# Optimization experiments

Hardware: AMD Instinct MI355X
Metric: run time of the kernel (lower is better)

The kernel has to match this reference:

```python
import jax, jax.numpy as jnp
import numpy as np
from jax import lax

NUM_ENT = 100000
NUM_REL = 500
ENT_DIM = 100   # emb_dim1 * emb_dim2 = 10 * 10
REL_DIM = 2500  # 100 filters * 5 * 5
BATCH = 1024
EPS = 1e-5


def _bn(x, gamma, beta, axes):
    # training-mode batchnorm (batch statistics), matching torch BN in train mode
    mean = jnp.mean(x, axis=axes, keepdims=True)
    var = jnp.var(x, axis=axes, keepdims=True)
    shape = [1] * x.ndim
    ch_axis = [a for a in range(x.ndim) if a not in axes][0]
    shape[ch_axis] = x.shape[ch_axis]
    g = gamma.reshape(shape)
    b = beta.reshape(shape)
    return (x - mean) * g * lax.rsqrt(var + EPS) + b


def setup_inputs() -> dict:
    key = jax.random.key(0)
    ks = jax.random.split(key, 6)
    e1 = jax.random.randint(ks[0], (BATCH,), 0, NUM_ENT)
    rel = jax.random.randint(ks[1], (BATCH,), 0, NUM_REL)
    emb_e = jax.random.normal(ks[2], (NUM_ENT, ENT_DIM), jnp.float32) * 0.1
    emb_rel = jax.random.normal(ks[3], (NUM_REL, REL_DIM), jnp.float32) * 0.1
    fc_w = jax.random.normal(ks[4], (ENT_DIM, 100 * 6 * 6), jnp.float32) * 0.02
    fc_b = jnp.zeros((ENT_DIM,), jnp.float32)
    bias = jnp.zeros((NUM_ENT,), jnp.float32)
    return {
        "e1": e1, "rel": rel,
        "emb_e": emb_e, "emb_rel": emb_rel,
        "fc_w": fc_w, "fc_b": fc_b, "bias": bias,
        "g0": jnp.ones((1,), jnp.float32), "b0": jnp.zeros((1,), jnp.float32),
        "g1": jnp.ones((100,), jnp.float32), "b1": jnp.zeros((100,), jnp.float32),
        "grel": jnp.ones((REL_DIM,), jnp.float32), "brel": jnp.zeros((REL_DIM,), jnp.float32),
        "g2": jnp.ones((ENT_DIM,), jnp.float32), "b2": jnp.zeros((ENT_DIM,), jnp.float32),
    }


def reference(e1, rel, emb_e, emb_rel, fc_w, fc_b, bias, g0, b0, g1, b1, grel, brel, g2, b2):
    B = e1.shape[0]
    e = emb_e[e1].reshape(B, 1, 10, 10)          # [B,1,10,10]
    r = emb_rel[rel]                              # [B,2500]
    r = _bn(r, grel, brel, axes=(0,))
    e = _bn(e, g0, b0, axes=(0, 2, 3))
    # dropout layers are identity (inference)
    filters = r.reshape(B * 100, 1, 5, 5)         # per-sample dynamic filters
    # per-sample conv as a single grouped conv: groups = B
    x = lax.conv_general_dilated(
        e.reshape(1, B, 10, 10), filters,
        window_strides=(1, 1), padding='VALID',
        feature_group_count=B,
        dimension_numbers=('NCHW', 'OIHW', 'NCHW'))
    x = x.reshape(B, 100, 6, 6)
    x = jax.nn.relu(_bn(x, g1, b1, axes=(0, 2, 3)))
    x = x.reshape(B, -1) @ fc_w.T + fc_b          # [B,100]
    x = jax.nn.relu(_bn(x, g2, b2, axes=(0,)))
    logits = x @ emb_e.T + bias                   # [B,NUM_ENT] memory-bound
    return jax.nn.sigmoid(logits)
```

## Files before the change

### kernel.cpp

```cpp
#include <hip/hip_runtime.h>
#include <cstdint>

#define NENT 100000
#define EPS 1e-5f

constexpr long REL_A    = 0;
constexpr long REL_B    = 2500;
constexpr long EPART    = 5000;
constexpr long EAB      = 5040;
constexpr long A1O      = 5056;
constexpr long C1O      = 5156;
constexpr long PART_OFF = 5888;
constexpr long XBUF_OFF = 415488;
constexpr long XHAT_OFF = 4101888;
constexpr long PSTAT    = XBUF_OFF;

typedef __attribute__((ext_vector_type(8))) __bf16 bf16x8;
typedef __attribute__((ext_vector_type(4))) float  f32x4;

#define BARLK() asm volatile("s_waitcnt lgkmcnt(0)\n\ts_barrier" ::: "memory")

__device__ __forceinline__ unsigned short f2bf(float f) {
    unsigned int u = __float_as_uint(f);
    unsigned int r = (u + 0x7FFFu + ((u >> 16) & 1u)) >> 16;
    return (unsigned short)r;
}

__global__ void k_stats1(const int* __restrict__ rel, const float* __restrict__ emb_rel,
                         const int* __restrict__ e1, const float* __restrict__ emb_e,
                         float* __restrict__ ws) {
    __shared__ float shmem[512];
    int tid = threadIdx.x, blk = blockIdx.x;
    if (blk < 125) {
        int* cnti = (int*)shmem;
        for (int i = tid; i < 512; i += 256) cnti[i] = 0;
        __syncthreads();
        for (int i = tid; i < 1024; i += 256) atomicAdd(&cnti[rel[i]], 1);
        __syncthreads();
        float s[10], q[10];
#pragma unroll
        for (int k = 0; k < 10; k++) { s[k] = 0.f; q[k] = 0.f; }
#pragma unroll
        for (int rr = 0; rr < 4; rr++) {
            int r = blk * 4 + rr;
            float c = (float)cnti[r];
            if (c != 0.f) {
                const float* row = emb_rel + (long)r * 2500;
#pragma unroll
                for (int k = 0; k < 10; k++) {
                    int idx = tid + k * 256;
                    if (idx < 2500) {
                        float v = row[idx];
                        s[k] = fmaf(c, v, s[k]);
                        q[k] = fmaf(c * v, v, q[k]);
                    }
                }
            }
        }
        float* ps = ws + PSTAT + (long)blk * 5000;
#pragma unroll
        for (int k = 0; k < 10; k++) {
            int idx = tid + k * 256;
            if (idx < 2500) { ps[idx] = s[k]; ps[2500 + idx] = q[k]; }
        }
    } else if (blk < 141) {
        float* ps = shmem;
        __shared__ float pq[256];
        __shared__ int eidx[64];
        int bi = blk - 125;
        if (tid < 64) eidx[tid] = e1[bi * 64 + tid];
        __syncthreads();
        float s = 0.f, q = 0.f;
        for (int i = tid; i < 6400; i += 256) {
            int b = i / 100, d = i - b * 100;
            float v = emb_e[(long)eidx[b] * 100 + d];
            s += v; q += v * v;
        }
        ps[tid] = s; pq[tid] = q;
        __syncthreads();
        for (int off = 128; off > 0; off >>= 1) {
            if (tid < off) { ps[tid] += ps[tid + off]; pq[tid] += pq[tid + off]; }
            __syncthreads();
        }
        if (tid == 0) { ws[EPART + bi * 2] = ps[0]; ws[EPART + bi * 2 + 1] = pq[0]; }
    }
}

__global__ void k_stats2(const float* __restrict__ grel, const float* __restrict__ brel,
                         const float* __restrict__ g0, const float* __restrict__ b0,
                         float* __restrict__ ws) {
    __shared__ float ps[512], pq[512];
    int tid = threadIdx.x, blk = blockIdx.x;
    if (blk < 40) {
        int f = blk * 64 + (tid & 63);
        int g = tid >> 6;
        float s = 0.f, q = 0.f;
        for (int p = g; p < 125; p += 8) {
            s += ws[PSTAT + (long)p * 5000 + f];
            q += ws[PSTAT + (long)p * 5000 + 2500 + f];
        }
        ps[tid] = s; pq[tid] = q;
        __syncthreads();
        if (tid < 64) {
            float ss = 0.f, qq = 0.f;
#pragma unroll
            for (int k = 0; k < 8; k++) { ss += ps[tid + k * 64]; qq += pq[tid + k * 64]; }
            float mean = ss * (1.f / 1024.f);
            float var  = qq * (1.f / 1024.f) - mean * mean;
            float a = grel[f] * rsqrtf(var + EPS);
            ws[REL_A + f] = a;
            ws[REL_B + f] = brel[f] - mean * a;
        }
    } else if (tid == 0) {
        float s = 0.f, q = 0.f;
#pragma unroll
        for (int i = 0; i < 16; i++) { s += ws[EPART + 2 * i]; q += ws[EPART + 2 * i + 1]; }
        float mean = s * (1.f / 102400.f);
        float var  = q * (1.f / 102400.f) - mean * mean;
        float a = g0[0] * rsqrtf(var + EPS);
        ws[EAB]     = a;
        ws[EAB + 1] = b0[0] - mean * a;
    }
}

__global__ void k_conv(const int* __restrict__ e1, const int* __restrict__ rel,
                       const float* __restrict__ emb_e, const float* __restrict__ emb_rel,
                       const float* __restrict__ ws, float* __restrict__ xout,
                       float* __restrict__ bn1part) {
    __shared__ float es[100];
    __shared__ float flt[2500];
    __shared__ float prs[600], prq[600];
    int b = blockIdx.x, tid = threadIdx.x;
    float a0 = ws[EAB], c0 = ws[EAB + 1];
    long ebase = (long)e1[b] * 100;
    for (int i = tid; i < 100; i += 256) es[i] = a0 * emb_e[ebase + i] + c0;
    long rbase = (long)rel[b] * 2500;
    for (int i = tid; i < 2500; i += 256) flt[i] = ws[REL_A + i] * emb_rel[rbase + i] + ws[REL_B + i];
    __syncthreads();
    for (int u = tid; u < 600; u += 256) {
        int f = u / 6, oi = u - f * 6;
        float er[5][10];
#pragma unroll
        for (int p = 0; p < 5; p++)
#pragma unroll
            for (int c = 0; c < 10; c++) er[p][c] = es[(oi + p) * 10 + c];
        float fw[25];
#pragma unroll
        for (int k = 0; k < 25; k++) fw[k] = flt[f * 25 + k];
        float* dst = xout + (long)b * 3600 + f * 36 + oi * 6;
        float s6 = 0.f, q6 = 0.f;
#pragma unroll
        for (int oj = 0; oj < 6; oj++) {
            float acc = 0.f;
#pragma unroll
            for (int p = 0; p < 5; p++)
#pragma unroll
                for (int q = 0; q < 5; q++) acc += er[p][oj + q] * fw[p * 5 + q];
            dst[oj] = acc;
            s6 += acc; q6 = fmaf(acc, acc, q6);
        }
        prs[u] = s6; prq[u] = q6;
    }
    __syncthreads();
    if (tid < 100) {
        float s = 0.f, q = 0.f;
#pragma unroll
        for (int k = 0; k < 6; k++) { s += prs[tid * 6 + k]; q += prq[tid * 6 + k]; }
        bn1part[(long)b * 200 + tid]       = s;
        bn1part[(long)b * 200 + 100 + tid] = q;
    }
}

__global__ void k_bn1r(const float* __restrict__ bn1part, const float* __restrict__ g1,
                       const float* __restrict__ b1, float* __restrict__ ws) {
    __shared__ float ps[256], pq[256];
    int f = blockIdx.x, tid = threadIdx.x;
    float s = 0.f, q = 0.f;
    for (int b = tid; b < 1024; b += 256) {
        s += bn1part[(long)b * 200 + f];
        q += bn1part[(long)b * 200 + 100 + f];
    }
    ps[tid] = s; pq[tid] = q;
    __syncthreads();
    for (int off = 128; off > 0; off >>= 1) {
        if (tid < off) { ps[tid] += ps[tid + off]; pq[tid] += pq[tid + off]; }
        __syncthreads();
    }
    if (tid == 0) {
        float mean = ps[0] * (1.f / 36864.f);
        float var  = pq[0] * (1.f / 36864.f) - mean * mean;
        float a = g1[f] * rsqrtf(var + EPS);
        ws[A1O + f] = a;
        ws[C1O + f] = b1[f] - mean * a;
    }
}

__global__ void k_fc(const float* __restrict__ xbuf, const float* __restrict__ fc_w,
                     const float* __restrict__ ws, float* __restrict__ part) {
    __shared__ float a1s[100], c1s[100];
    __shared__ float xs[4][900];
    int tid = threadIdx.x;
    int sb = blockIdx.x, kc = blockIdx.y;
    if (tid < 100) { a1s[tid] = ws[A1O + tid]; c1s[tid] = ws[C1O + tid]; }
    __syncthreads();
    int b0s = sb * 4, k0 = kc * 900;
    for (int idx = tid; idx < 3600; idx += 256) {
        int s = idx / 900, k = idx - s * 900;
        int kg = k0 + k;
        int f = kg / 36;
        float v = xbuf[(long)(b0s + s) * 3600 + kg];
        v = a1s[f] * v + c1s[f];
        xs[s][k] = v > 0.f ? v : 0.f;
    }
    __syncthreads();
    if (tid < 200) {
        int j = tid % 100, sg = tid / 100;
        float acc0 = 0.f, acc1 = 0.f;
        const float4* wrow = (const float4*)(fc_w + (long)j * 3600 + k0);
        const float4* x0 = (const float4*)(&xs[sg][0]);
        const float4* x1 = (const float4*)(&xs[sg + 2][0]);
#pragma unroll 5
        for (int kk = 0; kk < 225; kk++) {
            float4 w4 = wrow[kk];
            float4 a4 = x0[kk], b4 = x1[kk];
            acc0 += w4.x * a4.x + w4.y * a4.y + w4.z * a4.z + w4.w * a4.w;
            acc1 += w4.x * b4.x + w4.y * b4.y + w4.z * b4.z + w4.w * b4.w;
        }
        part[((long)kc * 1024 + b0s + sg) * 100 + j]     = acc0;
        part[((long)kc * 1024 + b0s + sg + 2) * 100 + j] = acc1;
    }
}

__global__ void k_bn2x(const float* __restrict__ part, const float* __restrict__ fc_b,
                       const float* __restrict__ g2, const float* __restrict__ b2,
                       unsigned short* __restrict__ xhat) {
    int j = blockIdx.x, tid = threadIdx.x;
    if (j >= 100) {
        for (int t = 0; t < 4; t++) xhat[(long)(tid + t * 256) * 128 + j] = 0;
        return;
    }
    __shared__ float ps[256], pq[256];
    __shared__ float ab[2];
    float v[4];
    float s = 0.f, q = 0.f;
#pragma unroll
    for (int t = 0; t < 4; t++) {
        int b = tid + t * 256;
        float x = part[(long)b * 100 + j] + part[(long)(1024 + b) * 100 + j]
                + part[(long)(2048 + b) * 100 + j] + part[(long)(3072 + b) * 100 + j]
                + fc_b[j];
        v[t] = x; s += x; q += x * x;
    }
    ps[tid] = s; pq[tid] = q;
    __syncthreads();
    for (int off = 128; off > 0; off >>= 1) {
        if (tid < off) { ps[tid] += ps[tid + off]; pq[tid] += pq[tid + off]; }
        __syncthreads();
    }
    if (tid == 0) {
        float mean = ps[0] * (1.f / 1024.f);
        float var  = pq[0] * (1.f / 1024.f) - mean * mean;
        float a = g2[j] * rsqrtf(var + EPS);
        ab[0] = a; ab[1] = b2[j] - mean * a;
    }
    __syncthreads();
    float a = ab[0], c = ab[1];
#pragma unroll
    for (int t = 0; t < 4; t++) {
        float x = a * v[t] + c;
        x = x > 0.f ? x : 0.f;
        xhat[(long)(tid + t * 256) * 128 + j] = f2bf(x);
    }
}

__global__ void __launch_bounds__(256, 2)
k_gemm(const unsigned short* __restrict__ xhat, const float* __restrict__ emb_e,
       const float* __restrict__ bias, float* __restrict__ out) {
    __shared__ __align__(16) unsigned short Es[256 * 128];
    char* EsB = (char*)Es;
    int tid = threadIdx.x;
    int n0 = blockIdx.x * 256;

    {
        int r = tid;
        int g = n0 + r;
        unsigned int rowb = (unsigned)r * 256u;
        unsigned int sw = ((unsigned)r & 7u) << 4;
        ushort4 z; z.x = z.y = z.z = z.w = 0;
        if (g < NENT) {
            const float4* src = (const float4*)(emb_e + (long)g * 100);
#pragma unroll
            for (int i = 0; i < 25; i++) {
                float4 v = src[i];
                ushort4 h;
                h.x = f2bf(v.x); h.y = f2bf(v.y); h.z = f2bf(v.z); h.w = f2bf(v.w);
                *(ushort4*)(EsB + ((rowb + 8u * i) ^ sw)) = h;
            }
        } else {
#pragma unroll
            for (int i = 0; i < 25; i++) *(ushort4*)(EsB + ((rowb + 8u * i) ^ sw)) = z;
        }
#pragma unroll
        for (int zz = 0; zz < 7; zz++) *(ushort4*)(EsB + ((rowb + 200u + 8u * zz) ^ sw)) = z;
    }
    __syncthreads();

    int w = tid >> 6, l = tid & 63;
    int l15 = l & 15, l4 = l >> 4;

    bf16x8 Af[4][4];
#pragma unroll
    for (int fe = 0; fe < 4; fe++) {
        unsigned int r = (unsigned)(w * 64 + fe * 16 + l15);
        unsigned int base = r * 256u + (unsigned)(l4 * 16);
        unsigned int sw = (r & 7u) << 4;
#pragma unroll
        for (int ks = 0; ks < 4; ks++)
            Af[ks][fe] = *(const bf16x8*)(EsB + ((base + (unsigned)(ks * 64)) ^ sw));
    }
    BARLK();

    int colg = n0 + l * 4;
    bool colv = colg < NENT;
    f32x4 bb = colv ? *(const f32x4*)(bias + colg) : f32x4{0.f, 0.f, 0.f, 0.f};

    int xrow = l15 * 128 + l4 * 8;

    bf16x8 Bp[4];
#pragma unroll
    for (int fx = 0; fx < 4; fx++)
        Bp[fx] = *(const bf16x8*)(xhat + (long)(fx * 2048 + xrow));

    for (int chunk = 0; chunk < 16; ++chunk) {
        int m0 = chunk * 64;
        f32x4 acc[4][4];
#pragma unroll
        for (int fe = 0; fe < 4; fe++)
#pragma unroll
            for (int fx = 0; fx < 4; fx++) acc[fe][fx] = f32x4{0.f, 0.f, 0.f, 0.f};

#pragma unroll
        for (int fe = 0; fe < 4; fe++)
#pragma unroll
            for (int fx = 0; fx < 4; fx++)
                acc[fe][fx] = __builtin_amdgcn_mfma_f32_16x16x32_bf16(Af[0][fe], Bp[fx], acc[fe][fx], 0, 0, 0);

#pragma unroll
        for (int ks = 1; ks < 4; ++ks) {
            bf16x8 Bf[4];
#pragma unroll
            for (int fx = 0; fx < 4; fx++)
                Bf[fx] = *(const bf16x8*)(xhat + (long)(m0 * 128 + fx * 2048 + ks * 32 + xrow));
#pragma unroll
            for (int fe = 0; fe < 4; fe++)
#pragma unroll
                for (int fx = 0; fx < 4; fx++)
                    acc[fe][fx] = __builtin_amdgcn_mfma_f32_16x16x32_bf16(Af[ks][fe], Bf[fx], acc[fe][fx], 0, 0, 0);
        }

        if (chunk < 15) {
            int m0n = (chunk + 1) * 64;
#pragma unroll
            for (int fx = 0; fx < 4; fx++)
                Bp[fx] = *(const bf16x8*)(xhat + (long)(m0n * 128 + fx * 2048 + xrow));
        }

#pragma unroll
        for (int fe = 0; fe < 4; fe++) {
            unsigned int s = (unsigned)(w * 16 + fe * 4 + l4);
#pragma unroll
            for (int fx = 0; fx < 4; fx++) {
                unsigned int row = (unsigned)(fx * 16 + l15);
                *(f32x4*)(EsB + row * 1024u + ((s ^ (row & 7u)) * 16u)) = acc[fe][fx];
            }
        }
        BARLK();

#pragma unroll
        for (int pass = 0; pass < 16; pass++) {
            unsigned int row = (unsigned)(pass * 4 + w);
            f32x4 v = *(f32x4*)(EsB + row * 1024u + ((((unsigned)l) ^ (row & 7u)) * 16u));
            f32x4 o;
#pragma unroll
            for (int k = 0; k < 4; k++) {
                float x = v[k] + bb[k];
                float e = __builtin_amdgcn_exp2f(x * -1.44269504f);
                o[k] = __builtin_amdgcn_rcpf(1.0f + e);
            }
            if (colv)
                __builtin_nontemporal_store(o, (f32x4*)(out + (long)(m0 + row) * NENT + colg));
        }
        BARLK();
    }
}

extern "C" void kernel_launch(void* const* d_in, const int* in_sizes, int n_in,
                              void* d_out, int out_size, void* d_ws, size_t ws_size,
                              hipStream_t stream) {
    const int*   e1      = (const int*)d_in[0];
    const int*   rel     = (const int*)d_in[1];
    const float* emb_e   = (const float*)d_in[2];
    const float* emb_rel = (const float*)d_in[3];
    const float* fc_w    = (const float*)d_in[4];
    const float* fc_b    = (const float*)d_in[5];
    const float* bias    = (const float*)d_in[6];
    const float* g0      = (const float*)d_in[7];
    const float* b0      = (const float*)d_in[8];
    const float* g1      = (const float*)d_in[9];
    const float* b1      = (const float*)d_in[10];
    const float* grel    = (const float*)d_in[11];
    const float* brel    = (const float*)d_in[12];
    const float* g2      = (const float*)d_in[13];
    const float* b2      = (const float*)d_in[14];
    float* ws  = (float*)d_ws;
    float* out = (float*)d_out;

    hipLaunchKernelGGL(k_stats1, dim3(141), dim3(256), 0, stream, rel, emb_rel, e1, emb_e, ws);
    hipLaunchKernelGGL(k_stats2, dim3(41), dim3(512), 0, stream, grel, brel, g0, b0, ws);
    hipLaunchKernelGGL(k_conv, dim3(1024), dim3(256), 0, stream, e1, rel, emb_e, emb_rel,
                       ws, ws + XBUF_OFF, ws + PART_OFF);
    hipLaunchKernelGGL(k_bn1r, dim3(100), dim3(256), 0, stream, ws + PART_OFF, g1, b1, ws);
    hipLaunchKernelGGL(k_fc, dim3(256, 4), dim3(256), 0, stream, ws + XBUF_OFF, fc_w, ws, ws + PART_OFF);
    hipLaunchKernelGGL(k_bn2x, dim3(128), dim3(256), 0, stream, ws + PART_OFF, fc_b, g2, b2,
                       (unsigned short*)(ws + XHAT_OFF));
    hipLaunchKernelGGL(k_gemm, dim3(391), dim3(256), 0, stream,
                       (const unsigned short*)(ws + XHAT_OFF), emb_e, bias, out);
}
```

Before: 201.8 us.

## Restructure FC kernel for 8-sample tiles with coalesced weights and transposed partials

```diff
diff --git a/kernel.cpp b/kernel.cpp
--- a/kernel.cpp
+++ b/kernel.cpp
@@ -166,8 +166,8 @@
         float s = 0.f, q = 0.f;
 #pragma unroll
         for (int k = 0; k < 6; k++) { s += prs[tid * 6 + k]; q += prq[tid * 6 + k]; }
-        bn1part[(long)b * 200 + tid]       = s;
-        bn1part[(long)b * 200 + 100 + tid] = q;
+        bn1part[(long)tid * 1024 + b]         = s;
+        bn1part[(long)(100 + tid) * 1024 + b] = q;
     }
 }
 
@@ -177,8 +177,8 @@
     int f = blockIdx.x, tid = threadIdx.x;
     float s = 0.f, q = 0.f;
     for (int b = tid; b < 1024; b += 256) {
-        s += bn1part[(long)b * 200 + f];
-        q += bn1part[(long)b * 200 + 100 + f];
+        s += bn1part[(long)f * 1024 + b];
+        q += bn1part[(long)(100 + f) * 1024 + b];
     }
     ps[tid] = s; pq[tid] = q;
     __syncthreads();
@@ -198,13 +198,13 @@
 __global__ void k_fc(const float* __restrict__ xbuf, const float* __restrict__ fc_w,
                      const float* __restrict__ ws, float* __restrict__ part) {
     __shared__ float a1s[100], c1s[100];
-    __shared__ float xs[4][900];
+    __shared__ float xs[8][900];
     int tid = threadIdx.x;
     int sb = blockIdx.x, kc = blockIdx.y;
     if (tid < 100) { a1s[tid] = ws[A1O + tid]; c1s[tid] = ws[C1O + tid]; }
     __syncthreads();
-    int b0s = sb * 4, k0 = kc * 900;
-    for (int idx = tid; idx < 3600; idx += 256) {
+    int b0s = sb * 8, k0 = kc * 900;
+    for (int idx = tid; idx < 7200; idx += 256) {
         int s = idx / 900, k = idx - s * 900;
         int kg = k0 + k;
         int f = kg / 36;
@@ -213,21 +213,42 @@
         xs[s][k] = v > 0.f ? v : 0.f;
     }
     __syncthreads();
-    if (tid < 200) {
-        int j = tid % 100, sg = tid / 100;
-        float acc0 = 0.f, acc1 = 0.f;
-        const float4* wrow = (const float4*)(fc_w + (long)j * 3600 + k0);
-        const float4* x0 = (const float4*)(&xs[sg][0]);
-        const float4* x1 = (const float4*)(&xs[sg + 2][0]);
-#pragma unroll 5
-        for (int kk = 0; kk < 225; kk++) {
-            float4 w4 = wrow[kk];
-            float4 a4 = x0[kk], b4 = x1[kk];
-            acc0 += w4.x * a4.x + w4.y * a4.y + w4.z * a4.z + w4.w * a4.w;
-            acc1 += w4.x * b4.x + w4.y * b4.y + w4.z * b4.z + w4.w * b4.w;
-        }
-        part[((long)kc * 1024 + b0s + sg) * 100 + j]     = acc0;
-        part[((long)kc * 1024 + b0s + sg + 2) * 100 + j] = acc1;
+    int w = tid >> 6, l = tid & 63;
+    int g = l >> 4, ks16 = l & 15;
+    for (int t = 0; t < 7; t++) {
+        int grp = w + 4 * t;
+        if (grp >= 25) break;
+        int j = grp * 4 + g;
+        const float* wrow = fc_w + (long)j * 3600 + k0;
+        float acc[8];
+#pragma unroll
+        for (int s = 0; s < 8; s++) acc[s] = 0.f;
+#pragma unroll
+        for (int i = 0; i < 15; i++) {
+            int kk = ks16 + i * 16;
+            if (kk < 225) {
+                float4 w4 = *(const float4*)(wrow + kk * 4);
+#pragma unroll
+                for (int s = 0; s < 8; s++) {
+                    float4 x4 = *(const float4*)(&xs[s][kk * 4]);
+                    acc[s] += w4.x * x4.x + w4.y * x4.y + w4.z * x4.z + w4.w * x4.w;
+                }
+            }
+        }
+#pragma unroll
+        for (int s = 0; s < 8; s++) {
+            float v = acc[s];
+            v += __shfl_xor(v, 1);
+            v += __shfl_xor(v, 2);
+            v += __shfl_xor(v, 4);
+            v += __shfl_xor(v, 8);
+            acc[s] = v;
+        }
+#pragma unroll
+        for (int s = 0; s < 8; s++) {
+            if (ks16 == s)
+                part[((long)kc * 100 + j) * 1024 + b0s + s] = acc[s];
+        }
     }
 }
 
@@ -246,8 +267,8 @@
 #pragma unroll
     for (int t = 0; t < 4; t++) {
         int b = tid + t * 256;
-        float x = part[(long)b * 100 + j] + part[(long)(1024 + b) * 100 + j]
-                + part[(long)(2048 + b) * 100 + j] + part[(long)(3072 + b) * 100 + j]
+        float x = part[(long)j * 1024 + b] + part[(long)(100 + j) * 1024 + b]
+                + part[(long)(200 + j) * 1024 + b] + part[(long)(300 + j) * 1024 + b]
                 + fc_b[j];
         v[t] = x; s += x; q += x * x;
     }
@@ -420,7 +441,7 @@
     hipLaunchKernelGGL(k_conv, dim3(1024), dim3(256), 0, stream, e1, rel, emb_e, emb_rel,
                        ws, ws + XBUF_OFF, ws + PART_OFF);
     hipLaunchKernelGGL(k_bn1r, dim3(100), dim3(256), 0, stream, ws + PART_OFF, g1, b1, ws);
-    hipLaunchKernelGGL(k_fc, dim3(256, 4), dim3(256), 0, stream, ws + XBUF_OFF, fc_w, ws, ws + PART_OFF);
+    hipLaunchKernelGGL(k_fc, dim3(128, 4), dim3(256), 0, stream, ws + XBUF_OFF, fc_w, ws, ws + PART_OFF);
     hipLaunchKernelGGL(k_bn2x, dim3(128), dim3(256), 0, stream, ws + PART_OFF, fc_b, g2, b2,
                        (unsigned short*)(ws + XHAT_OFF));
     hipLaunchKernelGGL(k_gemm, dim3(391), dim3(256), 0, stream,
```

Result: faster. 162.8 us, median of 2 (-19.3%).
